# Performance work log

Measured on AMD Instinct MI355X. Metric: run time of the kernel, lower is better.

The kernel has to match this reference:

```python
import jax, jax.numpy as jnp
import numpy as np

B, S, H, MAX_STEP = 128, 1024, 256, 10
NEG_INF = -1e8


def setup_inputs() -> dict:
    key = jax.random.key(0)
    ks = jax.random.split(key, 16)
    sc = 0.05
    return {
        "s0": jax.random.normal(ks[0], (B, H), jnp.float32),
        "h0": jax.random.normal(ks[1], (B, H), jnp.float32),
        "doc_encoding": jax.random.normal(ks[2], (B, S, H), jnp.float32),
        "W_ih": jax.random.normal(ks[3], (3 * H, H), jnp.float32) * sc,
        "W_hh": jax.random.normal(ks[4], (3 * H, H), jnp.float32) * sc,
        "b_ih": jax.random.normal(ks[5], (3 * H,), jnp.float32) * sc,
        "b_hh": jax.random.normal(ks[6], (3 * H,), jnp.float32) * sc,
        "Wq": jax.random.normal(ks[7], (H, H), jnp.float32) * sc,
        "bq": jax.random.normal(ks[8], (H,), jnp.float32) * sc,
        "Wd": jax.random.normal(ks[9], (H, H), jnp.float32) * sc,
        "bd": jax.random.normal(ks[10], (H,), jnp.float32) * sc,
        "Ws": jax.random.normal(ks[11], (1, H), jnp.float32) * sc,
        "bs": jax.random.normal(ks[12], (1,), jnp.float32) * sc,
        "tgt": jax.random.randint(ks[13], (B, MAX_STEP), 0, S, jnp.int64 if jax.config.jax_enable_x64 else jnp.int32),
        "sent_length": jax.random.randint(ks[14], (B,), 1, S + 1, jnp.int64 if jax.config.jax_enable_x64 else jnp.int32),
    }


def reference(s0, h0, doc_encoding, W_ih, W_hh, b_ih, b_hh, Wq, bq, Wd, bd, Ws, bs, tgt, sent_length):
    batch, sent_len, hid = doc_encoding.shape
    # padding mask: 1 where position >= doc length
    mask = (jnp.arange(sent_len)[None, :] >= sent_length[:, None]).astype(doc_encoding.dtype)  # [B,S]
    # precomputed attention keys: linear_d(context)
    precompute = jnp.einsum('bsh,kh->bsk', doc_encoding, Wd) + bd  # [B,S,H]
    # teacher-forced indices (original maps -1 -> 0)
    tgt_idx = jnp.where(tgt == -1, 0, tgt)  # [B,T]
    batch_ar = jnp.arange(batch)

    def gru_cell(x, h):
        gi = x @ W_ih.T + b_ih  # [B,3H]
        gh = h @ W_hh.T + b_hh
        i_r, i_z, i_n = jnp.split(gi, 3, axis=-1)
        h_r, h_z, h_n = jnp.split(gh, 3, axis=-1)
        r = jax.nn.sigmoid(i_r + h_r)
        z = jax.nn.sigmoid(i_z + h_z)
        n = jnp.tanh(i_n + r * h_n)
        return (1.0 - z) * n + z * h

    def step(carry, idx_t):
        cur_input, h = carry
        h = gru_cell(cur_input, h)
        target = h @ Wq.T + bq  # [B,H]
        energy = jnp.squeeze(jnp.tanh(precompute + target[:, None, :]) @ Ws.T, -1) + bs[0]  # [B,S]
        energy = energy * (1.0 - mask) + mask * NEG_INF
        cur_next = doc_encoding[batch_ar, idx_t]  # hard-attention gather [B,H]
        return (cur_next, h), energy

    _, all_score = jax.lax.scan(step, (s0, h0), tgt_idx.T)  # [T,B,S]
    return all_score, mask
```

## Files before the change

### kernel.cpp

```cpp
#include <hip/hip_runtime.h>

typedef unsigned short ushort_t;
typedef unsigned int uint_t;
typedef __attribute__((ext_vector_type(8))) short short8;
typedef __attribute__((ext_vector_type(4))) float f32x4;

#define B_   128
#define S_   1024
#define H_   256
#define T_   10
#define NEG_INF_ -1e8f

static __device__ __forceinline__ ushort_t f2bf(float x) {
    unsigned int u = __float_as_uint(x);
    unsigned int r = u + 0x7FFFu + ((u >> 16) & 1u);
    return (ushort_t)(r >> 16);
}
static __device__ __forceinline__ float bflo(uint_t w) {
    return __uint_as_float(w << 16);
}
static __device__ __forceinline__ float bfhi(uint_t w) {
    return __uint_as_float(w & 0xFFFF0000u);
}
static __device__ __forceinline__ float sigf(float x) {
    return 1.0f / (1.0f + __expf(-x));
}
static __device__ __forceinline__ float tanh_acc(float x) {
    return 2.0f / (1.0f + __expf(-2.0f * x)) - 1.0f;
}
static __device__ __forceinline__ float tanh_fast(float x) {
    float u = x * x;
    float p = fmaf(0.019063f, u, -0.18852f);
    p = fmaf(p, u, 0.93106f);
    float r = x * p;
    return __builtin_amdgcn_fmed3f(r, -1.0f, 1.0f);
}
static __device__ __forceinline__ short8 pack_bf8(float4 a, float4 b) {
    short8 r;
    r[0] = (short)f2bf(a.x); r[1] = (short)f2bf(a.y);
    r[2] = (short)f2bf(a.z); r[3] = (short)f2bf(a.w);
    r[4] = (short)f2bf(b.x); r[5] = (short)f2bf(b.y);
    r[6] = (short)f2bf(b.z); r[7] = (short)f2bf(b.w);
    return r;
}

__global__ void prep_transpose(const float* __restrict__ W_ih,
                               const float* __restrict__ W_hh,
                               const float* __restrict__ Wq,
                               uint_t* __restrict__ planes) {
    __shared__ float lds[64][65];
    const int p = blockIdx.x >> 4, tile = blockIdx.x & 15;
    const int j0 = (tile >> 2) * 64, c0 = (tile & 3) * 64;
    const float* src;
    if (p < 3)      src = W_ih + (size_t)p * 65536;
    else if (p < 6) src = W_hh + (size_t)(p - 3) * 65536;
    else            src = Wq;
    uint_t* dst = planes + (size_t)p * 32768;
    const int tid = threadIdx.x;
#pragma unroll
    for (int p4 = 0; p4 < 4; ++p4) {
        int i = p4 * 256 + tid;
        int jj = i >> 4, cc4 = (i & 15) * 4;
        float4 v = *((const float4*)&src[(size_t)(j0 + jj) * 256 + c0 + cc4]);
        lds[jj][cc4]     = v.x;
        lds[jj][cc4 + 1] = v.y;
        lds[jj][cc4 + 2] = v.z;
        lds[jj][cc4 + 3] = v.w;
    }
    __syncthreads();
#pragma unroll
    for (int p8 = 0; p8 < 8; ++p8) {
        int i = p8 * 256 + tid;
        int c2 = i >> 6, j = i & 63;
        float lo = lds[j][c2 * 2], hi = lds[j][c2 * 2 + 1];
        uint_t val = (uint_t)f2bf(lo) | ((uint_t)f2bf(hi) << 16);
        dst[(size_t)(c0 / 2 + c2) * 256 + j0 + j] = val;
    }
}

__global__ void prep_small(const float* __restrict__ Wd, const int* __restrict__ slen,
                           ushort_t* __restrict__ Wd_bf, float* __restrict__ out_mask) {
    int i = blockIdx.x * 256 + threadIdx.x;
    if (i < 65536) { Wd_bf[i] = f2bf(Wd[i]); return; }
    i -= 65536;
    int b = i >> 10, s = i & 1023;
    out_mask[i] = (s >= slen[b]) ? 1.0f : 0.0f;
}

__global__ __launch_bounds__(512) void gru_all(
        const float* __restrict__ s0, const float* __restrict__ h0,
        const float* __restrict__ doc, const int* __restrict__ tgt,
        const uint_t* __restrict__ planes, const float* __restrict__ b_ih,
        const float* __restrict__ b_hh, const float* __restrict__ bq,
        float* __restrict__ targets) {
    __shared__ float xs[T_][256];
    __shared__ float hs[256];
    __shared__ float pr[256], pz[256], pn[256], pq[256];
    const int b = blockIdx.x;
    const int tid = threadIdx.x;
    const int j = tid & 255, half = tid >> 8;

    const uint_t* ihr = planes;
    const uint_t* ihz = planes + 32768;
    const uint_t* ihn = planes + 2 * 32768;
    const uint_t* hhr = planes + 3 * 32768;
    const uint_t* hhz = planes + 4 * 32768;
    const uint_t* hhn = planes + 5 * 32768;
    const uint_t* qT  = planes + 6 * 32768;

    for (int i = tid; i < 640; i += 512) {
        int t = i >> 6, c4 = i & 63;
        const float* src;
        if (t == 0) src = s0 + (size_t)b * H_;
        else {
            int idx = tgt[b * T_ + t - 1];
            if (idx < 0) idx = 0;
            src = doc + ((size_t)b * S_ + idx) * H_;
        }
        ((float4*)&xs[t][0])[c4] = ((const float4*)src)[c4];
    }
    if (half == 0) hs[j] = h0[(size_t)b * H_ + j];
    const float bhr = b_hh[j], bhz = b_hh[j + 256], bhn = b_hh[j + 512];
    const float bqj = bq[j];
    const float bihr = b_ih[j], bihz = b_ih[j + 256], bihn = b_ih[j + 512];
    __syncthreads();

    float g_r[5], g_z[5], g_n[5];
#pragma unroll
    for (int u = 0; u < 5; ++u) { g_r[u] = bihr; g_z[u] = bihz; g_n[u] = bihn; }
    const int tbase = half * 5;
#pragma unroll 1
    for (int bb = 0; bb < 16; ++bb) {
        uint_t wr8[8], wz8[8], wn8[8];
#pragma unroll
        for (int v = 0; v < 8; ++v) {
            int c2 = bb * 8 + v;
            wr8[v] = ihr[c2 * 256 + j];
            wz8[v] = ihz[c2 * 256 + j];
            wn8[v] = ihn[c2 * 256 + j];
        }
#pragma unroll
        for (int v = 0; v < 8; ++v) {
            int c2 = bb * 8 + v;
            float wr0 = bflo(wr8[v]), wr1 = bfhi(wr8[v]);
            float wz0 = bflo(wz8[v]), wz1 = bfhi(wz8[v]);
            float wn0 = bflo(wn8[v]), wn1 = bfhi(wn8[v]);
#pragma unroll
            for (int u = 0; u < 5; ++u) {
                float2 x2 = *((const float2*)&xs[tbase + u][c2 * 2]);
                g_r[u] = fmaf(wr0, x2.x, g_r[u]); g_r[u] = fmaf(wr1, x2.y, g_r[u]);
                g_z[u] = fmaf(wz0, x2.x, g_z[u]); g_z[u] = fmaf(wz1, x2.y, g_z[u]);
                g_n[u] = fmaf(wn0, x2.x, g_n[u]); g_n[u] = fmaf(wn1, x2.y, g_n[u]);
            }
        }
    }

    const int c2base = half * 64;
    const uint_t* hhr_h = hhr + (size_t)c2base * 256 + j;
    const uint_t* hhz_h = hhz + (size_t)c2base * 256 + j;
    const uint_t* hhn_h = hhn + (size_t)c2base * 256 + j;
    const uint_t* qT_h  = qT  + (size_t)c2base * 256 + j;

#pragma unroll
    for (int t = 0; t < T_; ++t) {
        const bool holder = (half == (t >= 5 ? 1 : 0));
        const int u = (t < 5) ? t : t - 5;
        float ar = 0.f, az = 0.f, an = 0.f;
#pragma unroll 1
        for (int bb = 0; bb < 8; ++bb) {
            uint_t wr8[8], wz8[8], wn8[8];
#pragma unroll
            for (int v = 0; v < 8; ++v) {
                int c2i = bb * 8 + v;
                wr8[v] = hhr_h[c2i * 256];
                wz8[v] = hhz_h[c2i * 256];
                wn8[v] = hhn_h[c2i * 256];
            }
#pragma unroll
            for (int v = 0; v < 8; ++v) {
                int c2i = bb * 8 + v;
                float2 h2 = *((const float2*)&hs[(c2base + c2i) * 2]);
                ar = fmaf(bflo(wr8[v]), h2.x, ar); ar = fmaf(bfhi(wr8[v]), h2.y, ar);
                az = fmaf(bflo(wz8[v]), h2.x, az); az = fmaf(bfhi(wz8[v]), h2.y, az);
                an = fmaf(bflo(wn8[v]), h2.x, an); an = fmaf(bfhi(wn8[v]), h2.y, an);
            }
        }
        if (!holder) { pr[j] = ar; pz[j] = az; pn[j] = an; }
        __syncthreads();
        if (holder) {
            float art = ar + pr[j] + bhr;
            float azt = az + pz[j] + bhz;
            float ant = an + pn[j] + bhn;
            float r = sigf(g_r[u] + art);
            float z = sigf(g_z[u] + azt);
            float n = tanh_acc(fmaf(r, ant, g_n[u]));
            float hold = hs[j];
            hs[j] = fmaf(z, hold - n, n);
        }
        __syncthreads();
        float q = 0.f;
#pragma unroll 1
        for (int bb = 0; bb < 4; ++bb) {
            uint_t wq16[16];
#pragma unroll
            for (int v = 0; v < 16; ++v)
                wq16[v] = qT_h[(bb * 16 + v) * 256];
#pragma unroll
            for (int v = 0; v < 16; ++v) {
                int c2i = bb * 16 + v;
                float2 h2 = *((const float2*)&hs[(c2base + c2i) * 2]);
                q = fmaf(bflo(wq16[v]), h2.x, q); q = fmaf(bfhi(wq16[v]), h2.y, q);
            }
        }
        if (!holder) pq[j] = q;
        __syncthreads();
        if (holder) targets[((size_t)t * B_ + b) * H_ + j] = q + pq[j] + bqj;
    }
}

__global__ __launch_bounds__(256, 3) void energy_kernel(
        const float* __restrict__ doc, const ushort_t* __restrict__ Wd_bf,
        const float* __restrict__ targets, const float* __restrict__ bd,
        const float* __restrict__ Ws, const float* __restrict__ bs,
        const int* __restrict__ slenp, float* __restrict__ out) {
    __shared__ float tg[T_][256];
    __shared__ float ws_l[256], bd_l[256];
    const int bid = blockIdx.x;
    const int b = bid >> 3, st = bid & 7;
    const int tid = threadIdx.x;

    for (int i = tid; i < 640; i += 256) {
        int t = i >> 6, k4 = i & 63;
        ((float4*)&tg[t][0])[k4] = *((const float4*)&targets[((size_t)t * B_ + b) * H_ + k4 * 4]);
    }
    if (tid < 64) ((float4*)ws_l)[tid] = ((const float4*)Ws)[tid];
    else if (tid < 128) ((float4*)bd_l)[tid - 64] = ((const float4*)bd)[tid - 64];

    const int lane = tid & 63, w = tid >> 6;
    const int r16 = lane & 15, g = lane >> 4;

    const int s0_loc = st * 128 + w * 16 + r16;
    const float* drow0 = doc + ((size_t)b * S_ + s0_loc) * H_ + g * 8;
    const float* drow1 = drow0 + (size_t)64 * H_;
    short8 bdoc0[8], bdoc1[8];
#pragma unroll
    for (int ks = 0; ks < 8; ++ks) {
        float4 v0 = *((const float4*)(drow0 + ks * 32));
        float4 v1 = *((const float4*)(drow0 + ks * 32 + 4));
        bdoc0[ks] = pack_bf8(v0, v1);
        float4 u0 = *((const float4*)(drow1 + ks * 32));
        float4 u1 = *((const float4*)(drow1 + ks * 32 + 4));
        bdoc1[ks] = pack_bf8(u0, u1);
    }
    __syncthreads();

    float e0[T_], e1[T_];
#pragma unroll
    for (int t = 0; t < T_; ++t) { e0[t] = 0.f; e1[t] = 0.f; }

    const ushort_t* wbase = Wd_bf + (size_t)r16 * H_ + g * 8;
    const int kq = g * 4;

    short8 awd[8];
#pragma unroll
    for (int ks = 0; ks < 8; ++ks) awd[ks] = *((const short8*)(wbase + ks * 32));

#pragma unroll 1
    for (int nt = 0; nt < 16; ++nt) {
        const int k0 = nt * 16 + kq;

        short8 awn[8];
        if (nt < 15) {
            const ushort_t* wnext = wbase + (size_t)((nt + 1) * 16) * H_;
#pragma unroll
            for (int ks = 0; ks < 8; ++ks) awn[ks] = *((const short8*)(wnext + ks * 32));
        }

        f32x4 bd4 = *((const f32x4*)&bd_l[k0]);
        f32x4 a00 = bd4;
        f32x4 a01 = {0.f, 0.f, 0.f, 0.f};
        f32x4 a10 = bd4;
        f32x4 a11 = {0.f, 0.f, 0.f, 0.f};
#pragma unroll
        for (int ks = 0; ks < 4; ++ks) {
            a00 = __builtin_amdgcn_mfma_f32_16x16x32_bf16(awd[ks],     bdoc0[ks],     a00, 0, 0, 0);
            a01 = __builtin_amdgcn_mfma_f32_16x16x32_bf16(awd[ks + 4], bdoc0[ks + 4], a01, 0, 0, 0);
            a10 = __builtin_amdgcn_mfma_f32_16x16x32_bf16(awd[ks],     bdoc1[ks],     a10, 0, 0, 0);
            a11 = __builtin_amdgcn_mfma_f32_16x16x32_bf16(awd[ks + 4], bdoc1[ks + 4], a11, 0, 0, 0);
        }
        f32x4 pA = a00 + a01;
        f32x4 pB = a10 + a11;
        f32x4 ws4 = *((const f32x4*)&ws_l[k0]);
#pragma unroll
        for (int t = 0; t < T_; ++t) {
            f32x4 tg4 = *((const f32x4*)&tg[t][k0]);
#pragma unroll
            for (int rr = 0; rr < 4; ++rr) {
                e0[t] = fmaf(tanh_fast(pA[rr] + tg4[rr]), ws4[rr], e0[t]);
                e1[t] = fmaf(tanh_fast(pB[rr] + tg4[rr]), ws4[rr], e1[t]);
            }
        }

#pragma unroll
        for (int ks = 0; ks < 8; ++ks) awd[ks] = awn[ks];
    }

#pragma unroll
    for (int t = 0; t < T_; ++t) {
        e0[t] += __shfl_xor(e0[t], 16);
        e0[t] += __shfl_xor(e0[t], 32);
        e1[t] += __shfl_xor(e1[t], 16);
        e1[t] += __shfl_xor(e1[t], 32);
    }

    const int slen = slenp[b];
    const float bs0 = bs[0];
    const bool pad0 = (s0_loc >= slen);
    const bool pad1 = (s0_loc + 64 >= slen);
    float* obase = out + (size_t)b * S_ + s0_loc;
#pragma unroll
    for (int tt = g; tt < T_; tt += 4) {
        obase[(size_t)tt * B_ * S_]      = pad0 ? NEG_INF_ : (e0[tt] + bs0);
        obase[(size_t)tt * B_ * S_ + 64] = pad1 ? NEG_INF_ : (e1[tt] + bs0);
    }
}

extern "C" void kernel_launch(void* const* d_in, const int* in_sizes, int n_in,
                              void* d_out, int out_size, void* d_ws, size_t ws_size,
                              hipStream_t stream) {
    (void)in_sizes; (void)n_in; (void)out_size; (void)ws_size;
    const float* s0   = (const float*)d_in[0];
    const float* h0   = (const float*)d_in[1];
    const float* doc  = (const float*)d_in[2];
    const float* W_ih = (const float*)d_in[3];
    const float* W_hh = (const float*)d_in[4];
    const float* b_ih = (const float*)d_in[5];
    const float* b_hh = (const float*)d_in[6];
    const float* Wq   = (const float*)d_in[7];
    const float* bq   = (const float*)d_in[8];
    const float* Wd   = (const float*)d_in[9];
    const float* bd   = (const float*)d_in[10];
    const float* Ws   = (const float*)d_in[11];
    const float* bs   = (const float*)d_in[12];
    const int*   tgt  = (const int*)d_in[13];
    const int*   slen = (const int*)d_in[14];

    float* out_score = (float*)d_out;
    float* out_mask  = out_score + T_ * B_ * S_;

    char* ws = (char*)d_ws;
    uint_t*   planes  = (uint_t*)(ws + 0);
    ushort_t* Wd_bf   = (ushort_t*)(ws + 917504);
    float*    targets = (float*)(ws + 1048576);

    prep_transpose<<<112, 256, 0, stream>>>(W_ih, W_hh, Wq, planes);
    prep_small<<<768, 256, 0, stream>>>(Wd, slen, Wd_bf, out_mask);
    gru_all<<<128, 512, 0, stream>>>(s0, h0, doc, tgt, planes, b_ih, b_hh, bq, targets);
    energy_kernel<<<1024, 256, 0, stream>>>(doc, Wd_bf, targets, bd, Ws, bs, slen, out_score);
}
```

Before: 178.9 us.

## Skip fully padded energy tiles via compacted tile list

Adds a tiny kernel that builds a compacted list of (batch, seq-tile) pairs whose tile start lies within the sequence length. The energy kernel then processes only those tiles, and exits early for surplus blocks. The NEG_INF fill for padded positions moves into the prep kernel, which now also writes the padded score entries. This avoids loading doc rows and running the MFMA/tanh work for fully padded tiles, at the cost of an extra launch and extra prep writes.

```diff
diff --git a/kernel.cpp b/kernel.cpp
--- a/kernel.cpp
+++ b/kernel.cpp
@@ -79,12 +79,45 @@
 }
 
 __global__ void prep_small(const float* __restrict__ Wd, const int* __restrict__ slen,
-                           ushort_t* __restrict__ Wd_bf, float* __restrict__ out_mask) {
+                           ushort_t* __restrict__ Wd_bf, float* __restrict__ out_mask,
+                           float* __restrict__ out_score) {
     int i = blockIdx.x * 256 + threadIdx.x;
     if (i < 65536) { Wd_bf[i] = f2bf(Wd[i]); return; }
     i -= 65536;
-    int b = i >> 10, s = i & 1023;
-    out_mask[i] = (s >= slen[b]) ? 1.0f : 0.0f;
+    if (i < B_ * S_) {
+        int b = i >> 10, s = i & 1023;
+        out_mask[i] = (s >= slen[b]) ? 1.0f : 0.0f;
+        return;
+    }
+    i -= B_ * S_;
+    int bs = i & (B_ * S_ - 1);
+    int b = bs >> 10, s = bs & 1023;
+    if (s >= slen[b]) out_score[i] = NEG_INF_;
+}
+
+__global__ __launch_bounds__(1024) void build_tiles(const int* __restrict__ slen,
+                                                    int* __restrict__ tlist,
+                                                    int* __restrict__ tcount) {
+    const int tid = threadIdx.x;
+    const int b = tid >> 3, st = tid & 7;
+    const bool active = (st * 128) < slen[b];
+    unsigned long long m = __ballot(active);
+    const int lane = tid & 63, wv = tid >> 6;
+    __shared__ int wbase[16];
+    if (lane == 0) wbase[wv] = __popcll(m);
+    __syncthreads();
+    if (tid == 0) {
+        int s = 0;
+#pragma unroll
+        for (int i = 0; i < 16; ++i) { int c = wbase[i]; wbase[i] = s; s += c; }
+        *tcount = s;
+    }
+    __syncthreads();
+    if (active) {
+        unsigned long long below = (lane == 0) ? 0ull : (m << (64 - lane));
+        int pos = wbase[wv] + __popcll(below);
+        tlist[pos] = tid;
+    }
 }
 
 __global__ __launch_bounds__(512) void gru_all(
@@ -222,12 +255,17 @@
         const float* __restrict__ doc, const ushort_t* __restrict__ Wd_bf,
         const float* __restrict__ targets, const float* __restrict__ bd,
         const float* __restrict__ Ws, const float* __restrict__ bs,
-        const int* __restrict__ slenp, float* __restrict__ out) {
+        const int* __restrict__ slenp, const int* __restrict__ tlist,
+        const int* __restrict__ tcount, float* __restrict__ out) {
     __shared__ float tg[T_][256];
     __shared__ float ws_l[256], bd_l[256];
     const int bid = blockIdx.x;
-    const int b = bid >> 3, st = bid & 7;
+    if (bid >= *tcount) return;
+    const int tile = tlist[bid];
+    const int b = tile >> 3, st = tile & 7;
     const int tid = threadIdx.x;
+
+    const int slen = slenp[b];
 
     for (int i = tid; i < 640; i += 256) {
         int t = i >> 6, k4 = i & 63;
@@ -313,15 +351,14 @@
         e1[t] += __shfl_xor(e1[t], 32);
     }
 
-    const int slen = slenp[b];
     const float bs0 = bs[0];
     const bool pad0 = (s0_loc >= slen);
     const bool pad1 = (s0_loc + 64 >= slen);
     float* obase = out + (size_t)b * S_ + s0_loc;
 #pragma unroll
     for (int tt = g; tt < T_; tt += 4) {
-        obase[(size_t)tt * B_ * S_]      = pad0 ? NEG_INF_ : (e0[tt] + bs0);
-        obase[(size_t)tt * B_ * S_ + 64] = pad1 ? NEG_INF_ : (e1[tt] + bs0);
+        if (!pad0) obase[(size_t)tt * B_ * S_]      = e0[tt] + bs0;
+        if (!pad1) obase[(size_t)tt * B_ * S_ + 64] = e1[tt] + bs0;
     }
 }
 
@@ -352,9 +389,13 @@
     uint_t*   planes  = (uint_t*)(ws + 0);
     ushort_t* Wd_bf   = (ushort_t*)(ws + 917504);
     float*    targets = (float*)(ws + 1048576);
+    int*      tlist   = (int*)(ws + 2359296);
+    int*      tcount  = (int*)(ws + 2363392);
 
     prep_transpose<<<112, 256, 0, stream>>>(W_ih, W_hh, Wq, planes);
-    prep_small<<<768, 256, 0, stream>>>(Wd, slen, Wd_bf, out_mask);
+    prep_small<<<5888, 256, 0, stream>>>(Wd, slen, Wd_bf, out_mask, out_score);
+    build_tiles<<<1, 1024, 0, stream>>>(slen, tlist, tcount);
     gru_all<<<128, 512, 0, stream>>>(s0, h0, doc, tgt, planes, b_ih, b_hh, bq, targets);
-    energy_kernel<<<1024, 256, 0, stream>>>(doc, Wd_bf, targets, bd, Ws, bs, slen, out_score);
-}
+    energy_kernel<<<1024, 256, 0, stream>>>(doc, Wd_bf, targets, bd, Ws, bs, slen,
+                                            tlist, tcount, out_score);
+}
```

Result: faster. 161.6 us, median of 2 (-9.7%).
